# Kernel optimization log

Hardware: AMD Instinct MI355X
Metric: run time of the kernel (lower is better)

The kernel has to match this reference:

```python
import jax, jax.numpy as jnp
import numpy as np

N = 100000      # nodes
E = 3200000     # edges (avg degree 32)
D_IN = 128
H = 32          # hidden_dim
OUT = 8         # output_dim
EPS = 1e-5


def setup_inputs() -> dict:
    key = jax.random.key(0)
    ks = jax.random.split(key, 18)
    s = 0.05
    return {
        "x": jax.random.normal(ks[0], (N, D_IN), jnp.float32),
        "edge_index": jax.random.randint(ks[1], (2, E), 0, N, dtype=jnp.int32),
        # GCNConv weights (stored as [in, out]) and biases
        "W0": jax.random.normal(ks[2], (D_IN, H), jnp.float32) * s,
        "b0": jnp.zeros((H,), jnp.float32),
        "W1": jax.random.normal(ks[3], (H, H), jnp.float32) * s,
        "b1": jnp.zeros((H,), jnp.float32),
        "W2": jax.random.normal(ks[4], (H, H), jnp.float32) * s,
        "b2": jnp.zeros((H,), jnp.float32),
        # LayerNorms after layers 0 and 1 (num_layers-1 = 2 LNs)
        "ln0_g": jnp.ones((H,), jnp.float32),
        "ln0_b": jnp.zeros((H,), jnp.float32),
        "ln1_g": jnp.ones((H,), jnp.float32),
        "ln1_b": jnp.zeros((H,), jnp.float32),
        # post_mp: Linear(H, H//2) -> ReLU -> Linear(H//2, OUT)
        "mp_w1": jax.random.normal(ks[5], (H, H // 2), jnp.float32) * s,
        "mp_b1": jnp.zeros((H // 2,), jnp.float32),
        "mp_w2": jax.random.normal(ks[6], (H // 2, OUT), jnp.float32) * s,
        "mp_b2": jnp.zeros((OUT,), jnp.float32),
    }


def _layernorm(x, g, b):
    m = jnp.mean(x, axis=-1, keepdims=True)
    v = jnp.var(x, axis=-1, keepdims=True)
    return (x - m) * jax.lax.rsqrt(v + EPS) * g + b


def _gcn(x, W, bias, src, dst, norm):
    # GCNConv: theta(x) then normalized gather-scatter aggregation + bias
    h = x @ W                               # [N, out]
    msg = h[src] * norm[:, None]            # gather along edges
    out = jax.ops.segment_sum(msg, dst, num_segments=N)  # scatter-add
    return out + bias


def reference(x, edge_index, W0, b0, W1, b1, W2, b2,
              ln0_g, ln0_b, ln1_g, ln1_b, mp_w1, mp_b1, mp_w2, mp_b2):
    # add self-loops (PyG GCNConv default) and symmetric normalization
    loop = jnp.arange(N, dtype=edge_index.dtype)
    src = jnp.concatenate([edge_index[0], loop])
    dst = jnp.concatenate([edge_index[1], loop])
    deg = jax.ops.segment_sum(jnp.ones_like(dst, jnp.float32), dst, num_segments=N)
    dis = jnp.where(deg > 0, jax.lax.rsqrt(jnp.maximum(deg, 1.0)), 0.0)
    norm = dis[src] * dis[dst]              # [E+N]

    # dropout p=0.05 is inference-mode -> identity
    h = jax.nn.relu(_gcn(x, W0, b0, src, dst, norm))
    h = _layernorm(h, ln0_g, ln0_b)
    h = jax.nn.relu(_gcn(h, W1, b1, src, dst, norm))
    h = _layernorm(h, ln1_g, ln1_b)
    h = jax.nn.relu(_gcn(h, W2, b2, src, dst, norm))  # last layer: no LN

    # post_mp head
    h = jax.nn.relu(h @ mp_w1 + mp_b1)
    h = h @ mp_w2 + mp_b2
    return jax.nn.log_softmax(h, axis=1)
```

## Files before the change

### kernel.cpp

```cpp
#include <hip/hip_runtime.h>

#define NN 100000
#define NE 3200000
#define DIN 128
#define HD 32
#define MID 16
#define OUTD 8
#define LN_EPS 1e-5f

#define BINSHIFT 8
#define NB 391
#define CAP 10240
#define EPB 8192
#define ABS 1024
#define AITER (EPB / ABS)
#define CBS 1024


__device__ __forceinline__ float bf2f(unsigned short u) {
    union { unsigned int i; float f; } c;
    c.i = ((unsigned int)u) << 16;
    return c.f;
}
__device__ __forceinline__ unsigned short f2bf(float f) {
    union { float f; unsigned int i; } c;
    c.f = f;
    unsigned int r = c.i + 0x7FFFu + ((c.i >> 16) & 1u);
    return (unsigned short)(r >> 16);
}
__device__ __forceinline__ unsigned int pack2(float a, float b) {
    return (unsigned int)f2bf(a) | ((unsigned int)f2bf(b) << 16);
}
__device__ __forceinline__ void addpk(float& a0, float& a1, unsigned int u) {
    union { unsigned int i; float f; } lo, hi;
    lo.i = u << 16;
    hi.i = u & 0xFFFF0000u;
    a0 += lo.f;
    a1 += hi.f;
}


__global__ void k_zero_bins(int* __restrict__ g_bincur) {
    int i = blockIdx.x * blockDim.x + threadIdx.x;
    if (i < NB) g_bincur[i] = 0;
}

__global__ __launch_bounds__(ABS) void k_binA(const int* __restrict__ src,
                                              const int* __restrict__ dst,
                                              int* __restrict__ g_bincur,
                                              unsigned int* __restrict__ staged) {
    __shared__ int cnt[NB];
    __shared__ int base[NB];
    int tid = threadIdx.x;
    for (int t = tid; t < NB; t += ABS) cnt[t] = 0;
    __syncthreads();
    int e0 = blockIdx.x * EPB;
    int dreg[AITER];
#pragma unroll
    for (int i = 0; i < AITER; ++i) {
        int e = e0 + i * ABS + tid;
        dreg[i] = (e < NE) ? dst[e] : -1;
        if (dreg[i] >= 0) atomicAdd(&cnt[dreg[i] >> BINSHIFT], 1);
    }
    __syncthreads();
    for (int t = tid; t < NB; t += ABS) {
        int c = cnt[t];
        base[t] = c ? atomicAdd(&g_bincur[t], c) : 0;
        cnt[t] = 0;
    }
    __syncthreads();
#pragma unroll
    for (int i = 0; i < AITER; ++i) {
        int e = e0 + i * ABS + tid;
        int d = dreg[i];
        if (d >= 0) {
            int b = d >> BINSHIFT;
            int k = base[b] + atomicAdd(&cnt[b], 1);
            if (k < CAP)
                staged[(size_t)b * CAP + k] =
                    ((unsigned int)(d & 255) << 24) | (unsigned int)src[e];
        }
    }
}

__global__ void k_binscan(const int* __restrict__ g_bincur, int* __restrict__ g_binexcl,
                          int* __restrict__ row_ptr) {
    __shared__ int s[512];
    int v = (threadIdx.x < NB) ? min(g_bincur[threadIdx.x], CAP) : 0;
    s[threadIdx.x] = v;
    __syncthreads();
#pragma unroll
    for (int off = 1; off < 512; off <<= 1) {
        int t = (threadIdx.x >= off) ? s[threadIdx.x - off] : 0;
        __syncthreads();
        s[threadIdx.x] += t;
        __syncthreads();
    }
    if (threadIdx.x < NB) g_binexcl[threadIdx.x] = s[threadIdx.x] - v;
    if (threadIdx.x == NB - 1) row_ptr[NN] = s[threadIdx.x];
}

__global__ __launch_bounds__(CBS) void k_binC(const int* __restrict__ g_bincur,
                                              const int* __restrict__ g_binexcl,
                                              const unsigned int* __restrict__ staged,
                                              int* __restrict__ row_ptr,
                                              float* __restrict__ dis,
                                              int* __restrict__ csr_src) {
    __shared__ int cnt[256];
    __shared__ int scn[256];
    int b = blockIdx.x;
    int tid = threadIdx.x;
    int tot = min(g_bincur[b], CAP);
    if (tid < 256) cnt[tid] = 0;
    __syncthreads();
    const unsigned int* st = staged + (size_t)b * CAP;
    for (int i = tid; i < tot; i += CBS)
        atomicAdd(&cnt[st[i] >> 24], 1);
    __syncthreads();
    int v = 0;
    if (tid < 256) {
        v = cnt[tid];
        scn[tid] = v;
    }
    __syncthreads();
#pragma unroll
    for (int off = 1; off < 256; off <<= 1) {
        int t = (tid < 256 && tid >= off) ? scn[tid - off] : 0;
        __syncthreads();
        if (tid < 256) scn[tid] += t;
        __syncthreads();
    }
    int gbase = g_binexcl[b];
    if (tid < 256) {
        int excl = scn[tid] - v;
        int node = (b << BINSHIFT) + tid;
        if (node < NN) {
            row_ptr[node] = gbase + excl;
            dis[node] = rsqrtf((float)(v + 1));
        }
        cnt[tid] = excl;
    }
    __syncthreads();
    for (int i = tid; i < tot; i += CBS) {
        unsigned int p = st[i];
        int rank = atomicAdd(&cnt[p >> 24], 1);
        csr_src[gbase + rank] = (int)(p & 0xFFFFFFu);
    }
}


template <int K>
__global__ __launch_bounds__(256) void k_gemm(const float* __restrict__ x,
                                              const float* __restrict__ W,
                                              const float* __restrict__ dis,
                                              unsigned short* __restrict__ hs) {
    int lane = threadIdx.x & 63;
    int q = __builtin_amdgcn_readfirstlane(threadIdx.x >> 6);
    int n = blockIdx.x * 64 + lane;
    if (n >= NN) return;
    const float* xr = x + (size_t)n * K;
    const float* Wq = W + q * 8;
    float acc[8];
#pragma unroll
    for (int j = 0; j < 8; ++j) acc[j] = 0.f;
    for (int k0 = 0; k0 < K; k0 += 4) {
        float4 xv = *reinterpret_cast<const float4*>(xr + k0);
#pragma unroll
        for (int kk = 0; kk < 4; ++kk) {
            float xk = kk == 0 ? xv.x : kk == 1 ? xv.y : kk == 2 ? xv.z : xv.w;
#pragma unroll
            for (int j = 0; j < 8; ++j)
                acc[j] = fmaf(xk, Wq[(k0 + kk) * HD + j], acc[j]);
        }
    }
    float d = dis[n];
    uint4 p;
    p.x = pack2(acc[0] * d, acc[1] * d);
    p.y = pack2(acc[2] * d, acc[3] * d);
    p.z = pack2(acc[4] * d, acc[5] * d);
    p.w = pack2(acc[6] * d, acc[7] * d);
    *reinterpret_cast<uint4*>(hs + (size_t)n * HD + q * 8) = p;
}


template <int DO_LN>
__global__ void k_gather(const int* __restrict__ row_ptr, const int* __restrict__ csr_src,
                         const float* __restrict__ dis,
                         const unsigned short* __restrict__ h,
                         const float* __restrict__ bias,
                         const float* __restrict__ g, const float* __restrict__ bln,
                         float* __restrict__ out) {
    int idx = blockIdx.x * blockDim.x + threadIdx.x;
    int n = idx >> 3, sub = idx & 7;
    if (n >= NN) return;
    int c0 = sub << 2;

    uint2 u = *reinterpret_cast<const uint2*>(h + (size_t)n * HD + c0);
    float a0 = 0.f, a1 = 0.f, a2 = 0.f, a3 = 0.f;
    addpk(a0, a1, u.x);
    addpk(a2, a3, u.y);

    int e = row_ptr[n], end = row_ptr[n + 1];
    while (e < end && (e & 3)) {
        int s = csr_src[e];
        uint2 hv = *reinterpret_cast<const uint2*>(h + (size_t)s * HD + c0);
        addpk(a0, a1, hv.x);
        addpk(a2, a3, hv.y);
        ++e;
    }
    for (; e + 3 < end; e += 4) {
        int4 si = *reinterpret_cast<const int4*>(csr_src + e);
        uint2 h0 = *reinterpret_cast<const uint2*>(h + (size_t)si.x * HD + c0);
        uint2 h1 = *reinterpret_cast<const uint2*>(h + (size_t)si.y * HD + c0);
        uint2 h2 = *reinterpret_cast<const uint2*>(h + (size_t)si.z * HD + c0);
        uint2 h3 = *reinterpret_cast<const uint2*>(h + (size_t)si.w * HD + c0);
        addpk(a0, a1, h0.x); addpk(a2, a3, h0.y);
        addpk(a0, a1, h1.x); addpk(a2, a3, h1.y);
        addpk(a0, a1, h2.x); addpk(a2, a3, h2.y);
        addpk(a0, a1, h3.x); addpk(a2, a3, h3.y);
    }
    for (; e < end; ++e) {
        int s = csr_src[e];
        uint2 hv = *reinterpret_cast<const uint2*>(h + (size_t)s * HD + c0);
        addpk(a0, a1, hv.x);
        addpk(a2, a3, hv.y);
    }

    float d = dis[n];
    float4 bv = *reinterpret_cast<const float4*>(bias + c0);
    float v0 = fmaxf(fmaf(a0, d, bv.x), 0.f);
    float v1 = fmaxf(fmaf(a1, d, bv.y), 0.f);
    float v2 = fmaxf(fmaf(a2, d, bv.z), 0.f);
    float v3 = fmaxf(fmaf(a3, d, bv.w), 0.f);

    if (DO_LN) {
        float s = (v0 + v1) + (v2 + v3);
        float s2 = (v0 * v0 + v1 * v1) + (v2 * v2 + v3 * v3);
#pragma unroll
        for (int m = 4; m >= 1; m >>= 1) {
            s += __shfl_xor(s, m, 8);
            s2 += __shfl_xor(s2, m, 8);
        }
        float mean = s * (1.f / 32.f);
        float var = s2 * (1.f / 32.f) - mean * mean;
        float r = rsqrtf(var + LN_EPS);
        float4 gv = *reinterpret_cast<const float4*>(g + c0);
        float4 lb = *reinterpret_cast<const float4*>(bln + c0);
        v0 = (v0 - mean) * r * gv.x + lb.x;
        v1 = (v1 - mean) * r * gv.y + lb.y;
        v2 = (v2 - mean) * r * gv.z + lb.z;
        v3 = (v3 - mean) * r * gv.w + lb.w;
    }
    *reinterpret_cast<float4*>(out + (size_t)n * HD + c0) = make_float4(v0, v1, v2, v3);
}


__global__ void k_final(const float* __restrict__ hin,
                        const float* __restrict__ w1, const float* __restrict__ mb1,
                        const float* __restrict__ w2, const float* __restrict__ mb2,
                        float* __restrict__ out) {
    __shared__ float sw1[HD * MID], sw2[MID * OUTD], sb1[MID], sb2[OUTD];
    for (int t = threadIdx.x; t < HD * MID; t += blockDim.x) sw1[t] = w1[t];
    for (int t = threadIdx.x; t < MID * OUTD; t += blockDim.x) sw2[t] = w2[t];
    if (threadIdx.x < MID) sb1[threadIdx.x] = mb1[threadIdx.x];
    if (threadIdx.x < OUTD) sb2[threadIdx.x] = mb2[threadIdx.x];
    __syncthreads();
    int n = blockIdx.x * blockDim.x + threadIdx.x;
    if (n >= NN) return;
    float h[HD];
    const float* ar = hin + (size_t)n * HD;
#pragma unroll
    for (int k = 0; k < HD; ++k) h[k] = ar[k];
    float t[MID];
#pragma unroll
    for (int j = 0; j < MID; ++j) {
        float a = sb1[j];
#pragma unroll
        for (int k = 0; k < HD; ++k) a += h[k] * sw1[k * MID + j];
        t[j] = fmaxf(a, 0.f);
    }
    float o[OUTD];
#pragma unroll
    for (int j = 0; j < OUTD; ++j) {
        float a = sb2[j];
#pragma unroll
        for (int k = 0; k < MID; ++k) a += t[k] * sw2[k * OUTD + j];
        o[j] = a;
    }
    float mx = o[0];
#pragma unroll
    for (int j = 1; j < OUTD; ++j) mx = fmaxf(mx, o[j]);
    float se = 0.f;
#pragma unroll
    for (int j = 0; j < OUTD; ++j) se += __expf(o[j] - mx);
    float lse = __logf(se) + mx;
    float* orow = out + (size_t)n * OUTD;
#pragma unroll
    for (int j = 0; j < OUTD; ++j) orow[j] = o[j] - lse;
}


extern "C" void kernel_launch(void* const* d_in, const int* in_sizes, int n_in,
                              void* d_out, int out_size, void* d_ws, size_t ws_size,
                              hipStream_t stream) {
    const float* x     = (const float*)d_in[0];
    const int*   ei    = (const int*)d_in[1];
    const float* W0    = (const float*)d_in[2];
    const float* b0    = (const float*)d_in[3];
    const float* W1    = (const float*)d_in[4];
    const float* b1    = (const float*)d_in[5];
    const float* W2    = (const float*)d_in[6];
    const float* b2    = (const float*)d_in[7];
    const float* ln0_g = (const float*)d_in[8];
    const float* ln0_b = (const float*)d_in[9];
    const float* ln1_g = (const float*)d_in[10];
    const float* ln1_b = (const float*)d_in[11];
    const float* mp_w1 = (const float*)d_in[12];
    const float* mp_b1 = (const float*)d_in[13];
    const float* mp_w2 = (const float*)d_in[14];
    const float* mp_b2 = (const float*)d_in[15];
    float* out = (float*)d_out;

    const int* src = ei;
    const int* dst = ei + NE;

    char* w = (char*)d_ws;
    auto align256 = [](size_t v) { return (v + 255) & ~(size_t)255; };
    int* g_bincur  = (int*)w;   w += align256((size_t)NB * 4);
    int* g_binexcl = (int*)w;   w += align256((size_t)NB * 4);
    int* row_ptr   = (int*)w;   w += align256((size_t)(NN + 1) * 4);
    float* dis     = (float*)w; w += align256((size_t)NN * 4);
    char* uni = w;
    unsigned int* staged = (unsigned int*)uni;
    unsigned short* bufB = (unsigned short*)uni;
    float* bufA = (float*)(uni + align256((size_t)NN * HD * 2));
    size_t uni_sz = align256((size_t)NB * CAP * 4);
    size_t uni_sz2 = align256((size_t)NN * HD * 2) + align256((size_t)NN * HD * 4);
    w = uni + (uni_sz > uni_sz2 ? uni_sz : uni_sz2);
    int* csr_src = (int*)w;

    const int BS = 256;
    int gN  = (NN + BS - 1) / BS;
    int gA  = (NE + EPB - 1) / EPB;
    int gN8 = (NN * 8 + BS - 1) / BS;
    int gG  = (NN + 63) / 64;

    k_zero_bins<<<1, 512, 0, stream>>>(g_bincur);
    k_binA<<<gA, ABS, 0, stream>>>(src, dst, g_bincur, staged);
    k_binscan<<<1, 512, 0, stream>>>(g_bincur, g_binexcl, row_ptr);
    k_binC<<<NB, CBS, 0, stream>>>(g_bincur, g_binexcl, staged, row_ptr, dis, csr_src);

    k_gemm<DIN><<<gG, BS, 0, stream>>>(x, W0, dis, bufB);
    k_gather<1><<<gN8, BS, 0, stream>>>(row_ptr, csr_src, dis, bufB, b0,
                                        ln0_g, ln0_b, bufA);
    k_gemm<HD><<<gG, BS, 0, stream>>>(bufA, W1, dis, bufB);
    k_gather<1><<<gN8, BS, 0, stream>>>(row_ptr, csr_src, dis, bufB, b1,
                                        ln1_g, ln1_b, bufA);
    k_gemm<HD><<<gG, BS, 0, stream>>>(bufA, W2, dis, bufB);
    k_gather<0><<<gN8, BS, 0, stream>>>(row_ptr, csr_src, dis, bufB, b2,
                                        nullptr, nullptr, bufA);

    k_final<<<gN, BS, 0, stream>>>(bufA, mp_w1, mp_b1, mp_w2, mp_b2, out);
}
```

Baseline: 261.2 us.

## Split hidden features into two planar halves and gather each half separately

The GEMM now writes its bf16 output as two planar arrays of 16 features each, and the gather runs twice per layer, once per half, with 4 threads per node. Each half-table is 3.2 MB, so the random neighbour gathers should stay resident in L2/LLC instead of sweeping the full 6.4 MB table. Because one gather pass no longer sees all 32 features, LayerNorm moves into a separate kernel. That adds extra launches, a second read of row_ptr and csr_src per layer, and an extra read/write pass over the fp32 activations.

```diff
diff --git a/kernel.cpp b/kernel.cpp
--- a/kernel.cpp
+++ b/kernel.cpp
@@ -4,6 +4,7 @@
 #define NE 3200000
 #define DIN 128
 #define HD 32
+#define HHALF 16
 #define MID 16
 #define OUTD 8
 #define LN_EPS 1e-5f
@@ -179,23 +180,21 @@
     p.y = pack2(acc[2] * d, acc[3] * d);
     p.z = pack2(acc[4] * d, acc[5] * d);
     p.w = pack2(acc[6] * d, acc[7] * d);
-    *reinterpret_cast<uint4*>(hs + (size_t)n * HD + q * 8) = p;
-}
-
-
-template <int DO_LN>
-__global__ void k_gather(const int* __restrict__ row_ptr, const int* __restrict__ csr_src,
-                         const float* __restrict__ dis,
-                         const unsigned short* __restrict__ h,
-                         const float* __restrict__ bias,
-                         const float* __restrict__ g, const float* __restrict__ bln,
-                         float* __restrict__ out) {
+    *reinterpret_cast<uint4*>(hs + ((size_t)(q >> 1) * NN + n) * HHALF + (q & 1) * 8) = p;
+}
+
+
+__global__ __launch_bounds__(256) void k_gather_half(
+        const int* __restrict__ row_ptr, const int* __restrict__ csr_src,
+        const float* __restrict__ dis, const unsigned short* __restrict__ hh,
+        const float* __restrict__ bias, int half, float* __restrict__ out) {
     int idx = blockIdx.x * blockDim.x + threadIdx.x;
-    int n = idx >> 3, sub = idx & 7;
+    int n = idx >> 2, sub = idx & 3;
     if (n >= NN) return;
-    int c0 = sub << 2;
-
-    uint2 u = *reinterpret_cast<const uint2*>(h + (size_t)n * HD + c0);
+    int cl = sub << 2;
+    int c0 = half * HHALF + cl;
+
+    uint2 u = *reinterpret_cast<const uint2*>(hh + (size_t)n * HHALF + cl);
     float a0 = 0.f, a1 = 0.f, a2 = 0.f, a3 = 0.f;
     addpk(a0, a1, u.x);
     addpk(a2, a3, u.y);
@@ -203,17 +202,17 @@
     int e = row_ptr[n], end = row_ptr[n + 1];
     while (e < end && (e & 3)) {
         int s = csr_src[e];
-        uint2 hv = *reinterpret_cast<const uint2*>(h + (size_t)s * HD + c0);
+        uint2 hv = *reinterpret_cast<const uint2*>(hh + (size_t)s * HHALF + cl);
         addpk(a0, a1, hv.x);
         addpk(a2, a3, hv.y);
         ++e;
     }
     for (; e + 3 < end; e += 4) {
         int4 si = *reinterpret_cast<const int4*>(csr_src + e);
-        uint2 h0 = *reinterpret_cast<const uint2*>(h + (size_t)si.x * HD + c0);
-        uint2 h1 = *reinterpret_cast<const uint2*>(h + (size_t)si.y * HD + c0);
-        uint2 h2 = *reinterpret_cast<const uint2*>(h + (size_t)si.z * HD + c0);
-        uint2 h3 = *reinterpret_cast<const uint2*>(h + (size_t)si.w * HD + c0);
+        uint2 h0 = *reinterpret_cast<const uint2*>(hh + (size_t)si.x * HHALF + cl);
+        uint2 h1 = *reinterpret_cast<const uint2*>(hh + (size_t)si.y * HHALF + cl);
+        uint2 h2 = *reinterpret_cast<const uint2*>(hh + (size_t)si.z * HHALF + cl);
+        uint2 h3 = *reinterpret_cast<const uint2*>(hh + (size_t)si.w * HHALF + cl);
         addpk(a0, a1, h0.x); addpk(a2, a3, h0.y);
         addpk(a0, a1, h1.x); addpk(a2, a3, h1.y);
         addpk(a0, a1, h2.x); addpk(a2, a3, h2.y);
@@ -221,7 +220,7 @@
     }
     for (; e < end; ++e) {
         int s = csr_src[e];
-        uint2 hv = *reinterpret_cast<const uint2*>(h + (size_t)s * HD + c0);
+        uint2 hv = *reinterpret_cast<const uint2*>(hh + (size_t)s * HHALF + cl);
         addpk(a0, a1, hv.x);
         addpk(a2, a3, hv.y);
     }
@@ -232,26 +231,35 @@
     float v1 = fmaxf(fmaf(a1, d, bv.y), 0.f);
     float v2 = fmaxf(fmaf(a2, d, bv.z), 0.f);
     float v3 = fmaxf(fmaf(a3, d, bv.w), 0.f);
-
-    if (DO_LN) {
-        float s = (v0 + v1) + (v2 + v3);
-        float s2 = (v0 * v0 + v1 * v1) + (v2 * v2 + v3 * v3);
-#pragma unroll
-        for (int m = 4; m >= 1; m >>= 1) {
-            s += __shfl_xor(s, m, 8);
-            s2 += __shfl_xor(s2, m, 8);
-        }
-        float mean = s * (1.f / 32.f);
-        float var = s2 * (1.f / 32.f) - mean * mean;
-        float r = rsqrtf(var + LN_EPS);
-        float4 gv = *reinterpret_cast<const float4*>(g + c0);
-        float4 lb = *reinterpret_cast<const float4*>(bln + c0);
-        v0 = (v0 - mean) * r * gv.x + lb.x;
-        v1 = (v1 - mean) * r * gv.y + lb.y;
-        v2 = (v2 - mean) * r * gv.z + lb.z;
-        v3 = (v3 - mean) * r * gv.w + lb.w;
-    }
     *reinterpret_cast<float4*>(out + (size_t)n * HD + c0) = make_float4(v0, v1, v2, v3);
+}
+
+
+__global__ __launch_bounds__(256) void k_ln(float* __restrict__ buf,
+                                            const float* __restrict__ g,
+                                            const float* __restrict__ bln) {
+    int idx = blockIdx.x * blockDim.x + threadIdx.x;
+    int n = idx >> 3, sub = idx & 7;
+    if (n >= NN) return;
+    int c0 = sub << 2;
+    float4 v = *reinterpret_cast<float4*>(buf + (size_t)n * HD + c0);
+    float s = (v.x + v.y) + (v.z + v.w);
+    float s2 = (v.x * v.x + v.y * v.y) + (v.z * v.z + v.w * v.w);
+#pragma unroll
+    for (int m = 4; m >= 1; m >>= 1) {
+        s += __shfl_xor(s, m, 8);
+        s2 += __shfl_xor(s2, m, 8);
+    }
+    float mean = s * (1.f / 32.f);
+    float var = s2 * (1.f / 32.f) - mean * mean;
+    float r = rsqrtf(var + LN_EPS);
+    float4 gv = *reinterpret_cast<const float4*>(g + c0);
+    float4 lb = *reinterpret_cast<const float4*>(bln + c0);
+    v.x = (v.x - mean) * r * gv.x + lb.x;
+    v.y = (v.y - mean) * r * gv.y + lb.y;
+    v.z = (v.z - mean) * r * gv.z + lb.z;
+    v.w = (v.w - mean) * r * gv.w + lb.w;
+    *reinterpret_cast<float4*>(buf + (size_t)n * HD + c0) = v;
 }
 
 
@@ -331,9 +339,9 @@
     int* row_ptr   = (int*)w;   w += align256((size_t)(NN + 1) * 4);
     float* dis     = (float*)w; w += align256((size_t)NN * 4);
     char* uni = w;
-    unsigned int* staged = (unsigned int*)uni;
     unsigned short* bufB = (unsigned short*)uni;
     float* bufA = (float*)(uni + align256((size_t)NN * HD * 2));
+    unsigned int* staged = (unsigned int*)uni;
     size_t uni_sz = align256((size_t)NB * CAP * 4);
     size_t uni_sz2 = align256((size_t)NN * HD * 2) + align256((size_t)NN * HD * 4);
     w = uni + (uni_sz > uni_sz2 ? uni_sz : uni_sz2);
@@ -343,7 +351,11 @@
     int gN  = (NN + BS - 1) / BS;
     int gA  = (NE + EPB - 1) / EPB;
     int gN8 = (NN * 8 + BS - 1) / BS;
+    int gN4 = (NN * 4 + BS - 1) / BS;
     int gG  = (NN + 63) / 64;
+
+    unsigned short* h0 = bufB;
+    unsigned short* h1 = bufB + (size_t)NN * HHALF;
 
     k_zero_bins<<<1, 512, 0, stream>>>(g_bincur);
     k_binA<<<gA, ABS, 0, stream>>>(src, dst, g_bincur, staged);
@@ -351,14 +363,16 @@
     k_binC<<<NB, CBS, 0, stream>>>(g_bincur, g_binexcl, staged, row_ptr, dis, csr_src);
 
     k_gemm<DIN><<<gG, BS, 0, stream>>>(x, W0, dis, bufB);
-    k_gather<1><<<gN8, BS, 0, stream>>>(row_ptr, csr_src, dis, bufB, b0,
-                                        ln0_g, ln0_b, bufA);
+    k_gather_half<<<gN4, BS, 0, stream>>>(row_ptr, csr_src, dis, h0, b0, 0, bufA);
+    k_gather_half<<<gN4, BS, 0, stream>>>(row_ptr, csr_src, dis, h1, b0, 1, bufA);
+    k_ln<<<gN8, BS, 0, stream>>>(bufA, ln0_g, ln0_b);
     k_gemm<HD><<<gG, BS, 0, stream>>>(bufA, W1, dis, bufB);
-    k_gather<1><<<gN8, BS, 0, stream>>>(row_ptr, csr_src, dis, bufB, b1,
-                                        ln1_g, ln1_b, bufA);
+    k_gather_half<<<gN4, BS, 0, stream>>>(row_ptr, csr_src, dis, h0, b1, 0, bufA);
+    k_gather_half<<<gN4, BS, 0, stream>>>(row_ptr, csr_src, dis, h1, b1, 1, bufA);
+    k_ln<<<gN8, BS, 0, stream>>>(bufA, ln1_g, ln1_b);
     k_gemm<HD><<<gG, BS, 0, stream>>>(bufA, W2, dis, bufB);
-    k_gather<0><<<gN8, BS, 0, stream>>>(row_ptr, csr_src, dis, bufB, b2,
-                                        nullptr, nullptr, bufA);
+    k_gather_half<<<gN4, BS, 0, stream>>>(row_ptr, csr_src, dis, h0, b2, 0, bufA);
+    k_gather_half<<<gN4, BS, 0, stream>>>(row_ptr, csr_src, dis, h1, b2, 1, bufA);
 
     k_final<<<gN, BS, 0, stream>>>(bufA, mp_w1, mp_b1, mp_w2, mp_b2, out);
 }
```

After: 330.5 us. 1.27x slower.
